# Performance work log

Measured on AMD Instinct MI355X. Metric: run time of the kernel, lower is better.

## Reference

```python
import jax, jax.numpy as jnp
import numpy as np

DIM = 512
HEADS = 8


def setup_inputs() -> dict:
    key = jax.random.key(0)
    ks = jax.random.split(key, 9)
    s = 1.0 / np.sqrt(DIM)
    x = jax.random.normal(ks[0], (2, 4096, DIM), dtype=jnp.float32)
    Wq = jax.random.uniform(ks[1], (DIM, DIM), jnp.float32, -s, s)
    bq = jax.random.uniform(ks[2], (DIM,), jnp.float32, -s, s)
    Wk = jax.random.uniform(ks[3], (DIM, DIM), jnp.float32, -s, s)
    bk = jax.random.uniform(ks[4], (DIM,), jnp.float32, -s, s)
    Wv = jax.random.uniform(ks[5], (DIM, DIM), jnp.float32, -s, s)
    bv = jax.random.uniform(ks[6], (DIM,), jnp.float32, -s, s)
    Wo = jax.random.uniform(ks[7], (DIM, DIM), jnp.float32, -s, s)
    bo = jax.random.uniform(ks[8], (DIM,), jnp.float32, -s, s)
    return {"x": x, "Wq": Wq, "bq": bq, "Wk": Wk, "bk": bk,
            "Wv": Wv, "bv": bv, "Wo": Wo, "bo": bo}


def reference(x, Wq, bq, Wk, bk, Wv, bv, Wo, bo):
    b, t, d = x.shape
    h = HEADS
    dq = d // h
    scale = dq ** -0.5
    # projections: torch Linear is x @ W.T + b
    q = (x @ Wq.T + bq).reshape(b, t, h, dq)
    k = (x @ Wk.T + bk).reshape(b, t, h, dq)
    v = (x @ Wv.T + bv).reshape(b, t, h, dq)
    # attention scores [b, h, t, t] (full O(T^2) matrix, as in the original)
    att = jnp.einsum("bqhd,bkhd->bhqk", q, k) * scale
    att = jax.nn.softmax(att, axis=-1)
    out = jnp.einsum("bhqk,bkhd->bqhd", att, v).reshape(b, t, d)
    return out @ Wo.T + bo
```

## Files before the change

kernel.cpp:

```cpp
#include <hip/hip_runtime.h>

typedef short bf16x8 __attribute__((ext_vector_type(8)));
typedef float f32x4 __attribute__((ext_vector_type(4)));
typedef unsigned u32x2 __attribute__((ext_vector_type(2)));
typedef unsigned u32x4 __attribute__((ext_vector_type(4)));

#define MFMA(a, b, c) __builtin_amdgcn_mfma_f32_16x16x32_bf16((a), (b), (c), 0, 0, 0)

__device__ __forceinline__ unsigned cvtpk(float a, float b) {
    unsigned r;
    asm("v_cvt_pk_bf16_f32 %0, %1, %2" : "=v"(r) : "v"(a), "v"(b));
    return r;
}

__device__ __forceinline__ void gload16(const void* g, void* l) {
    __builtin_amdgcn_global_load_lds(
        (const __attribute__((address_space(1))) unsigned*)g,
        (__attribute__((address_space(3))) unsigned*)l, 16, 0, 0);
}

__global__ __launch_bounds__(256) void cvt_kernel(
    const float* __restrict__ x,
    const float* __restrict__ w0, const float* __restrict__ w1,
    const float* __restrict__ w2, const float* __restrict__ w3,
    unsigned short* __restrict__ xd,
    unsigned short* __restrict__ d0, unsigned short* __restrict__ d1,
    unsigned short* __restrict__ d2, unsigned short* __restrict__ d3)
{
    int bid = blockIdx.x;
    const float* src;
    unsigned short* dst;
    int off;
    if (bid < 4096) { src = x; dst = xd; off = bid; }
    else {
        int s = (bid - 4096) >> 8;
        src = s == 0 ? w0 : (s == 1 ? w1 : (s == 2 ? w2 : w3));
        dst = s == 0 ? d0 : (s == 1 ? d1 : (s == 2 ? d2 : d3));
        off = (bid - 4096) & 255;
    }
    size_t i = ((size_t)off * 256 + threadIdx.x) * 4;
    float4 v = *(const float4*)(src + i);
    uint2 pk;
    pk.x = cvtpk(v.x, v.y);
    pk.y = cvtpk(v.z, v.w);
    *(uint2*)(dst + i) = pk;
}

__global__ __launch_bounds__(512, 6) void qkv_kernel(
    const unsigned short* __restrict__ x,
    const unsigned short* __restrict__ Wq, const float* __restrict__ bq,
    const unsigned short* __restrict__ Wk, const float* __restrict__ bk,
    const unsigned short* __restrict__ Wv, const float* __restrict__ bv,
    unsigned short* __restrict__ qo, unsigned short* __restrict__ ko,
    unsigned short* __restrict__ vo)
{
    __shared__ unsigned short sA[128 * 64];
    __shared__ unsigned short sB[128 * 64];
    const int tid = threadIdx.x;
    const int lane = tid & 63, wid = tid >> 6;
    const int quad = lane >> 4, l15 = lane & 15;
    const int wm = wid >> 2, wn = wid & 3;
    const int by = blockIdx.y;
    const int sel = by >> 2;
    const int n0 = (by & 3) * 128;
    const int m0 = blockIdx.x * 128;
    const unsigned short* W = sel == 0 ? Wq : (sel == 1 ? Wk : Wv);
    const float* bias = sel == 0 ? bq : (sel == 1 ? bk : bv);

    const int gl_r = lane >> 3;
    const int gl_kc = (lane & 7) ^ gl_r;

    f32x4 acc[4][2];
    #pragma unroll
    for (int i = 0; i < 4; i++)
        #pragma unroll
        for (int j = 0; j < 2; j++) {
            f32x4 z = {0.f, 0.f, 0.f, 0.f};
            acc[i][j] = z;
        }

    for (int k0 = 0; k0 < 512; k0 += 64) {
        #pragma unroll
        for (int p = 0; p < 2; p++) {
            int chunk = wid * 2 + p;
            int row = chunk * 8 + gl_r;
            gload16(x + (size_t)(m0 + row) * 512 + k0 + gl_kc * 8,
                    (char*)sA + chunk * 1024);
            gload16(W + (size_t)(n0 + row) * 512 + k0 + gl_kc * 8,
                    (char*)sB + chunk * 1024);
        }
        __asm__ __volatile__("s_waitcnt vmcnt(0)" ::: "memory");
        __syncthreads();
        #pragma unroll
        for (int ks = 0; ks < 2; ks++) {
            bf16x8 af[4], bfr[2];
            #pragma unroll
            for (int i = 0; i < 4; i++) {
                int row = wm * 64 + i * 16 + l15;
                int kc = ks * 4 + quad;
                af[i] = *(const bf16x8*)((const char*)sA + row * 128 + ((kc ^ (row & 7)) << 4));
            }
            #pragma unroll
            for (int j = 0; j < 2; j++) {
                int row = wn * 32 + j * 16 + l15;
                int kc = ks * 4 + quad;
                bfr[j] = *(const bf16x8*)((const char*)sB + row * 128 + ((kc ^ (row & 7)) << 4));
            }
            #pragma unroll
            for (int i = 0; i < 4; i++)
                #pragma unroll
                for (int j = 0; j < 2; j++)
                    acc[i][j] = MFMA(af[i], bfr[j], acc[i][j]);
        }
        __syncthreads();
    }

    float bv2[2];
    #pragma unroll
    for (int j = 0; j < 2; j++) bv2[j] = bias[n0 + wn * 32 + j * 16 + l15];

    if (sel != 1) {
        const float SC = (sel == 0) ? 0.125f * 1.44269504088896f : 1.0f;
        unsigned short* dstT = (sel == 0) ? qo : vo;
        #pragma unroll
        for (int i = 0; i < 4; i++) {
            #pragma unroll
            for (int j = 0; j < 2; j++) {
                int n = n0 + wn * 32 + j * 16 + l15;
                int h = n >> 6, d = n & 63;
                int m = m0 + wm * 64 + i * 16 + quad * 4;
                int b = m >> 12, t = m & 4095;
                uint2 pk;
                pk.x = cvtpk((acc[i][j][0] + bv2[j]) * SC,
                             (acc[i][j][1] + bv2[j]) * SC);
                pk.y = cvtpk((acc[i][j][2] + bv2[j]) * SC,
                             (acc[i][j][3] + bv2[j]) * SC);
                *(uint2*)(dstT + ((size_t)(b * 8 + h) * 64 + d) * 4096 + t) = pk;
            }
        }
    } else {
        #pragma unroll
        for (int i = 0; i < 4; i++) {
            #pragma unroll
            for (int j = 0; j < 2; j++) {
                int n = n0 + wn * 32 + j * 16 + l15;
                int h = n >> 6, d = n & 63;
                int m = m0 + wm * 64 + i * 16 + quad * 4;
                int b = m >> 12, t = m & 4095;
                size_t base2 = ((size_t)(b * 8 + h) * 4096 + t) * 64 + d;
                unsigned p01 = cvtpk(acc[i][j][0] + bv2[j], acc[i][j][1] + bv2[j]);
                unsigned p23 = cvtpk(acc[i][j][2] + bv2[j], acc[i][j][3] + bv2[j]);
                ko[base2]       = (unsigned short)p01;
                ko[base2 + 64]  = (unsigned short)(p01 >> 16);
                ko[base2 + 128] = (unsigned short)p23;
                ko[base2 + 192] = (unsigned short)(p23 >> 16);
            }
        }
    }
}

__global__ __launch_bounds__(512, 4) void attn_kernel(
    const unsigned short* __restrict__ qg, const unsigned short* __restrict__ kg,
    const unsigned short* __restrict__ vtg, unsigned short* __restrict__ og)
{
    __shared__ unsigned char smem[66048];

    const int tid = threadIdx.x;
    const int lane = tid & 63;
    const int w = tid >> 6;
    const int g = tid >> 8;
    const int wg = w & 3;
    const int sw = w & 3;
    const int quad = lane >> 4, l15 = lane & 15;
    const int bh = blockIdx.y;
    const size_t base = (size_t)bh * 4096 * 64;
    const unsigned short* Q = qg + base;
    const unsigned short* K = kg + base;
    const unsigned short* VT = vtg + base;
    const int qt0 = blockIdx.x * 128;

    const int srow = lane >> 3;
    const int skc  = (lane & 7) ^ srow;

    int kLaneOff[2], vLaneOff[2], dKOff[2], dVOff[2];
    #pragma unroll
    for (int p = 0; p < 2; p++) {
        int chunk = wg * 2 + p;
        int row = chunk * 8 + srow;
        kLaneOff[p] = row * 64 + skc * 8;
        vLaneOff[p] = row * 4096 + skc * 8;
        dKOff[p] = g * 8192 + chunk * 1024;
        dVOff[p] = 16384 + g * 8192 + chunk * 1024;
    }

    int okS[4][2], okV[4][2];
    #pragma unroll
    for (int rb = 0; rb < 4; rb++)
        #pragma unroll
        for (int ks = 0; ks < 2; ks++) {
            int row = rb * 16 + l15;
            int kc = ks * 4 + quad;
            int sl = ((kc ^ (row & 7)) << 4);
            okS[rb][ks] = g * 8192 + row * 128 + sl;
            okV[rb][ks] = 16384 + g * 8192 + row * 128 + sl;
        }

    bf16x8 qf[2][2];
    #pragma unroll
    for (int cb = 0; cb < 2; cb++) {
        int t = qt0 + sw * 32 + cb * 16 + l15;
        #pragma unroll
        for (int ks = 0; ks < 2; ks++) {
            bf16x8 v;
            #pragma unroll
            for (int e = 0; e < 8; e++)
                v[e] = (short)Q[(size_t)(ks * 32 + quad * 8 + e) * 4096 + t];
            qf[cb][ks] = v;
        }
    }

    f32x4 ot[4][2];
    #pragma unroll
    for (int i = 0; i < 4; i++)
        #pragma unroll
        for (int cb = 0; cb < 2; cb++) {
            f32x4 z = {0.f, 0.f, 0.f, 0.f};
            ot[i][cb] = z;
        }
    f32x4 ls[2];
    {
        f32x4 z = {0.f, 0.f, 0.f, 0.f};
        ls[0] = z; ls[1] = z;
    }
    const short one_b = (short)0x3F80;
    const bf16x8 ones = {one_b, one_b, one_b, one_b, one_b, one_b, one_b, one_b};

    {
        int kb = g * 64;
        #pragma unroll
        for (int p = 0; p < 2; p++) {
            gload16(K + (size_t)kb * 64 + kLaneOff[p], smem + dKOff[p]);
            gload16(VT + (size_t)kb + vLaneOff[p], smem + dVOff[p]);
        }
    }

    auto do_iter = [&](int it, int bufoff) {
        __asm__ __volatile__("s_waitcnt vmcnt(0)" ::: "memory");
        __syncthreads();

        if (it < 31) {
            int kb = (2 * (it + 1) + g) * 64;
            int od = bufoff ^ 32768;
            #pragma unroll
            for (int p = 0; p < 2; p++) {
                gload16(K + (size_t)kb * 64 + kLaneOff[p], smem + od + dKOff[p]);
                gload16(VT + (size_t)kb + vLaneOff[p], smem + od + dVOff[p]);
            }
        }

        #pragma unroll
        for (int half = 0; half < 2; half++) {
            unsigned xA[2], yA[2], zB[2], wB[2];
            #pragma unroll
            for (int rb2 = 0; rb2 < 2; rb2++) {
                int rb = half * 2 + rb2;
                f32x4 s0 = {0.f, 0.f, 0.f, 0.f};
                f32x4 s1 = {0.f, 0.f, 0.f, 0.f};
                __builtin_amdgcn_s_setprio(1);
                #pragma unroll
                for (int ks = 0; ks < 2; ks++) {
                    bf16x8 ka = *(const bf16x8*)(smem + bufoff + okS[rb][ks]);
                    s0 = MFMA(ka, qf[0][ks], s0);
                    s1 = MFMA(ka, qf[1][ks], s1);
                }
                __builtin_amdgcn_s_setprio(0);
                unsigned e0 = cvtpk(__builtin_amdgcn_exp2f(s0[0]),
                                    __builtin_amdgcn_exp2f(s0[1]));
                unsigned e1 = cvtpk(__builtin_amdgcn_exp2f(s0[2]),
                                    __builtin_amdgcn_exp2f(s0[3]));
                unsigned f0 = cvtpk(__builtin_amdgcn_exp2f(s1[0]),
                                    __builtin_amdgcn_exp2f(s1[1]));
                unsigned f1 = cvtpk(__builtin_amdgcn_exp2f(s1[2]),
                                    __builtin_amdgcn_exp2f(s1[3]));
                if (rb2 == 0) { xA[0] = e0; yA[0] = e1; xA[1] = f0; yA[1] = f1; }
                else          { zB[0] = e0; wB[0] = e1; zB[1] = f0; wB[1] = f1; }
            }

            bf16x8 pf[2];
            #pragma unroll
            for (int cb = 0; cb < 2; cb++) {
                u32x2 s  = __builtin_amdgcn_permlane32_swap(xA[cb], zB[cb], false, false);
                u32x2 t  = __builtin_amdgcn_permlane16_swap(s[0], s[1], false, false);
                u32x2 s2 = __builtin_amdgcn_permlane32_swap(yA[cb], wB[cb], false, false);
                u32x2 t2 = __builtin_amdgcn_permlane16_swap(s2[0], s2[1], false, false);
                u32x4 fr = { t[0], t2[0], t[1], t2[1] };
                pf[cb] = __builtin_bit_cast(bf16x8, fr);
            }

            __builtin_amdgcn_s_setprio(1);
            ls[0] = MFMA(ones, pf[0], ls[0]);
            ls[1] = MFMA(ones, pf[1], ls[1]);
            #pragma unroll
            for (int rbd = 0; rbd < 4; rbd++) {
                bf16x8 vf = *(const bf16x8*)(smem + bufoff + okV[rbd][half]);
                ot[rbd][0] = MFMA(vf, pf[0], ot[rbd][0]);
                ot[rbd][1] = MFMA(vf, pf[1], ot[rbd][1]);
            }
            __builtin_amdgcn_s_setprio(0);
        }
    };

    for (int it2 = 0; it2 < 16; it2++) {
        do_iter(2 * it2, 0);
        do_iter(2 * it2 + 1, 32768);
    }

    float* oc = (float*)smem;
    float* lc = (float*)(smem + 65536);
    if (g == 1) {
        #pragma unroll
        for (int cb = 0; cb < 2; cb++) {
            int qb = sw * 32 + cb * 16 + l15;
            if (quad == 0) lc[qb] = ls[cb][0];
            #pragma unroll
            for (int rbd = 0; rbd < 4; rbd++) {
                int dc = rbd * 4 + quad;
                *(f32x4*)((char*)oc + qb * 256 + ((dc ^ (qb & 15)) << 4)) = ot[rbd][cb];
            }
        }
    }
    __syncthreads();
    if (g == 0) {
        const int b = bh >> 3, h = bh & 7;
        #pragma unroll
        for (int cb = 0; cb < 2; cb++) {
            int qb = sw * 32 + cb * 16 + l15;
            float inv = 1.f / (ls[cb][0] + lc[qb]);
            int q = qt0 + qb;
            #pragma unroll
            for (int rbd = 0; rbd < 4; rbd++) {
                int dc = rbd * 4 + quad;
                f32x4 o2 = *(const f32x4*)((char*)oc + qb * 256 + ((dc ^ (qb & 15)) << 4));
                uint2 pk;
                pk.x = cvtpk((ot[rbd][cb][0] + o2[0]) * inv,
                             (ot[rbd][cb][1] + o2[1]) * inv);
                pk.y = cvtpk((ot[rbd][cb][2] + o2[2]) * inv,
                             (ot[rbd][cb][3] + o2[3]) * inv);
                *(uint2*)(og + ((size_t)(b * 4096 + q) * 512 + h * 64 + rbd * 16 + quad * 4)) = pk;
            }
        }
    }
}

__global__ __launch_bounds__(256) void out_kernel(
    const unsigned short* __restrict__ attn,
    const unsigned short* __restrict__ Wo, const float* __restrict__ bo,
    float* __restrict__ out)
{
    __shared__ unsigned short sA[64 * 64];
    __shared__ unsigned short sB[64 * 64];
    const int tid = threadIdx.x;
    const int lane = tid & 63, wid = tid >> 6;
    const int quad = lane >> 4, l15 = lane & 15;
    const int wm = wid >> 1, wn = wid & 1;
    const int m0 = blockIdx.x * 64;
    const int n0 = blockIdx.y * 64;

    const int gl_r = lane >> 3;
    const int gl_kc = (lane & 7) ^ gl_r;

    f32x4 acc[2][2];
    #pragma unroll
    for (int i = 0; i < 2; i++)
        #pragma unroll
        for (int j = 0; j < 2; j++) {
            f32x4 z = {0.f, 0.f, 0.f, 0.f};
            acc[i][j] = z;
        }

    for (int k0 = 0; k0 < 512; k0 += 64) {
        #pragma unroll
        for (int p = 0; p < 2; p++) {
            int chunk = wid * 2 + p;
            int row = chunk * 8 + gl_r;
            gload16(attn + (size_t)(m0 + row) * 512 + k0 + gl_kc * 8,
                    (char*)sA + chunk * 1024);
            gload16(Wo + (size_t)(n0 + row) * 512 + k0 + gl_kc * 8,
                    (char*)sB + chunk * 1024);
        }
        __asm__ __volatile__("s_waitcnt vmcnt(0)" ::: "memory");
        __syncthreads();
        #pragma unroll
        for (int ks = 0; ks < 2; ks++) {
            bf16x8 af[2], bfr[2];
            #pragma unroll
            for (int i = 0; i < 2; i++) {
                int row = wm * 32 + i * 16 + l15;
                int kc = ks * 4 + quad;
                af[i] = *(const bf16x8*)((const char*)sA + row * 128 + ((kc ^ (row & 7)) << 4));
            }
            #pragma unroll
            for (int j = 0; j < 2; j++) {
                int row = wn * 32 + j * 16 + l15;
                int kc = ks * 4 + quad;
                bfr[j] = *(const bf16x8*)((const char*)sB + row * 128 + ((kc ^ (row & 7)) << 4));
            }
            #pragma unroll
            for (int i = 0; i < 2; i++)
                #pragma unroll
                for (int j = 0; j < 2; j++)
                    acc[i][j] = MFMA(af[i], bfr[j], acc[i][j]);
        }
        __syncthreads();
    }

    float bv2[2];
    #pragma unroll
    for (int j = 0; j < 2; j++) bv2[j] = bo[n0 + wn * 32 + j * 16 + l15];
    #pragma unroll
    for (int i = 0; i < 2; i++) {
        #pragma unroll
        for (int j = 0; j < 2; j++) {
            int n = n0 + wn * 32 + j * 16 + l15;
            #pragma unroll
            for (int r = 0; r < 4; r++) {
                int m = m0 + wm * 32 + i * 16 + quad * 4 + r;
                out[(size_t)m * 512 + n] = acc[i][j][r] + bv2[j];
            }
        }
    }
}

extern "C" void kernel_launch(void* const* d_in, const int* in_sizes, int n_in,
                              void* d_out, int out_size, void* d_ws, size_t ws_size,
                              hipStream_t stream) {
    const float* x  = (const float*)d_in[0];
    const float* Wq = (const float*)d_in[1];
    const float* bq = (const float*)d_in[2];
    const float* Wk = (const float*)d_in[3];
    const float* bk = (const float*)d_in[4];
    const float* Wv = (const float*)d_in[5];
    const float* bv = (const float*)d_in[6];
    const float* Wo = (const float*)d_in[7];
    const float* bo = (const float*)d_in[8];
    unsigned short* ws = (unsigned short*)d_ws;

    const size_t NTOK = (size_t)2 * 4096 * 512;
    const size_t WSZ = (size_t)512 * 512;
    unsigned short* xb  = ws;
    unsigned short* Wqb = ws + NTOK;
    unsigned short* Wkb = Wqb + WSZ;
    unsigned short* Wvb = Wkb + WSZ;
    unsigned short* Wob = Wvb + WSZ;
    unsigned short* q_ws = Wob + WSZ;
    unsigned short* k_ws = q_ws + NTOK;
    unsigned short* v_ws = k_ws + NTOK;
    unsigned short* a_ws = v_ws + NTOK;

    cvt_kernel<<<5120, 256, 0, stream>>>(x, Wq, Wk, Wv, Wo, xb, Wqb, Wkb, Wvb, Wob);
    qkv_kernel<<<dim3(64, 12), 512, 0, stream>>>(xb, Wqb, bq, Wkb, bk, Wvb, bv,
                                                 q_ws, k_ws, v_ws);
    attn_kernel<<<dim3(32, 16), 512, 0, stream>>>(q_ws, k_ws, v_ws, a_ws);
    out_kernel<<<dim3(128, 8), 256, 0, stream>>>(a_ws, Wob, bo,
                                                 (float*)d_out);
}
```

Measured before the change: 186.0 us.

## Restructure attention to 64-query blocks without split-KV reduction

The attention kernel moves from 512-thread blocks that split the key range across two warp groups, each with two 16-query tiles per warp, to 256-thread blocks that handle 64 queries and loop over all 64 key blocks. Each warp now owns a single 16-query tile. This drops the shared-memory cross-group reduction and its extra barrier, halves LDS use, and doubles the grid so more blocks can be resident. In exchange, K/V tiles are reused across half as many queries per load, which doubles K/V traffic from L2/LDS, and each warp has less independent MFMA work to hide latency.

```diff
diff --git a/kernel.cpp b/kernel.cpp
--- a/kernel.cpp
+++ b/kernel.cpp
@@ -159,25 +159,22 @@
     }
 }
 
-__global__ __launch_bounds__(512, 4) void attn_kernel(
+__global__ __launch_bounds__(256, 4) void attn_kernel(
     const unsigned short* __restrict__ qg, const unsigned short* __restrict__ kg,
     const unsigned short* __restrict__ vtg, unsigned short* __restrict__ og)
 {
-    __shared__ unsigned char smem[66048];
+    __shared__ unsigned char smem[32768];
 
     const int tid = threadIdx.x;
     const int lane = tid & 63;
     const int w = tid >> 6;
-    const int g = tid >> 8;
-    const int wg = w & 3;
-    const int sw = w & 3;
     const int quad = lane >> 4, l15 = lane & 15;
     const int bh = blockIdx.y;
     const size_t base = (size_t)bh * 4096 * 64;
     const unsigned short* Q = qg + base;
     const unsigned short* K = kg + base;
     const unsigned short* VT = vtg + base;
-    const int qt0 = blockIdx.x * 128;
+    const int qt0 = blockIdx.x * 64;
 
     const int srow = lane >> 3;
     const int skc  = (lane & 7) ^ srow;
@@ -185,12 +182,12 @@
     int kLaneOff[2], vLaneOff[2], dKOff[2], dVOff[2];
     #pragma unroll
     for (int p = 0; p < 2; p++) {
-        int chunk = wg * 2 + p;
+        int chunk = w * 2 + p;
         int row = chunk * 8 + srow;
         kLaneOff[p] = row * 64 + skc * 8;
         vLaneOff[p] = row * 4096 + skc * 8;
-        dKOff[p] = g * 8192 + chunk * 1024;
-        dVOff[p] = 16384 + g * 8192 + chunk * 1024;
+        dKOff[p] = chunk * 1024;
+        dVOff[p] = 8192 + chunk * 1024;
     }
 
     int okS[4][2], okV[4][2];
@@ -199,58 +196,56 @@
         #pragma unroll
         for (int ks = 0; ks < 2; ks++) {
             int row = rb * 16 + l15;
-            int kc = ks * 4 + quad;
-            int sl = ((kc ^ (row & 7)) << 4);
-            okS[rb][ks] = g * 8192 + row * 128 + sl;
-            okV[rb][ks] = 16384 + g * 8192 + row * 128 + sl;
-        }
-
-    bf16x8 qf[2][2];
-    #pragma unroll
-    for (int cb = 0; cb < 2; cb++) {
-        int t = qt0 + sw * 32 + cb * 16 + l15;
+            okS[rb][ks] = row * 128 + (((ks * 4 + quad) ^ (row & 7)) << 4);
+        }
+    #pragma unroll
+    for (int rbd = 0; rbd < 4; rbd++)
+        #pragma unroll
+        for (int half = 0; half < 2; half++) {
+            int row = rbd * 16 + l15;
+            okV[rbd][half] = 8192 + row * 128 + (((half * 4 + quad) ^ (row & 7)) << 4);
+        }
+
+    bf16x8 qf[2];
+    {
+        int t = qt0 + w * 16 + l15;
         #pragma unroll
         for (int ks = 0; ks < 2; ks++) {
             bf16x8 v;
             #pragma unroll
             for (int e = 0; e < 8; e++)
                 v[e] = (short)Q[(size_t)(ks * 32 + quad * 8 + e) * 4096 + t];
-            qf[cb][ks] = v;
-        }
-    }
-
-    f32x4 ot[4][2];
-    #pragma unroll
-    for (int i = 0; i < 4; i++)
-        #pragma unroll
-        for (int cb = 0; cb < 2; cb++) {
-            f32x4 z = {0.f, 0.f, 0.f, 0.f};
-            ot[i][cb] = z;
-        }
-    f32x4 ls[2];
+            qf[ks] = v;
+        }
+    }
+
+    f32x4 ot[4];
+    #pragma unroll
+    for (int i = 0; i < 4; i++) {
+        f32x4 z = {0.f, 0.f, 0.f, 0.f};
+        ot[i] = z;
+    }
+    f32x4 ls;
     {
         f32x4 z = {0.f, 0.f, 0.f, 0.f};
-        ls[0] = z; ls[1] = z;
+        ls = z;
     }
     const short one_b = (short)0x3F80;
     const bf16x8 ones = {one_b, one_b, one_b, one_b, one_b, one_b, one_b, one_b};
 
-    {
-        int kb = g * 64;
-        #pragma unroll
-        for (int p = 0; p < 2; p++) {
-            gload16(K + (size_t)kb * 64 + kLaneOff[p], smem + dKOff[p]);
-            gload16(VT + (size_t)kb + vLaneOff[p], smem + dVOff[p]);
-        }
+    #pragma unroll
+    for (int p = 0; p < 2; p++) {
+        gload16(K + kLaneOff[p], smem + dKOff[p]);
+        gload16(VT + vLaneOff[p], smem + dVOff[p]);
     }
 
     auto do_iter = [&](int it, int bufoff) {
         __asm__ __volatile__("s_waitcnt vmcnt(0)" ::: "memory");
         __syncthreads();
 
-        if (it < 31) {
-            int kb = (2 * (it + 1) + g) * 64;
-            int od = bufoff ^ 32768;
+        if (it < 63) {
+            int kb = (it + 1) * 64;
+            int od = bufoff ^ 16384;
             #pragma unroll
             for (int p = 0; p < 2; p++) {
                 gload16(K + (size_t)kb * 64 + kLaneOff[p], smem + od + dKOff[p]);
@@ -260,94 +255,59 @@
 
         #pragma unroll
         for (int half = 0; half < 2; half++) {
-            unsigned xA[2], yA[2], zB[2], wB[2];
+            unsigned xA, yA, zB, wB;
             #pragma unroll
             for (int rb2 = 0; rb2 < 2; rb2++) {
                 int rb = half * 2 + rb2;
                 f32x4 s0 = {0.f, 0.f, 0.f, 0.f};
-                f32x4 s1 = {0.f, 0.f, 0.f, 0.f};
                 __builtin_amdgcn_s_setprio(1);
                 #pragma unroll
                 for (int ks = 0; ks < 2; ks++) {
                     bf16x8 ka = *(const bf16x8*)(smem + bufoff + okS[rb][ks]);
-                    s0 = MFMA(ka, qf[0][ks], s0);
-                    s1 = MFMA(ka, qf[1][ks], s1);
+                    s0 = MFMA(ka, qf[ks], s0);
                 }
                 __builtin_amdgcn_s_setprio(0);
                 unsigned e0 = cvtpk(__builtin_amdgcn_exp2f(s0[0]),
                                     __builtin_amdgcn_exp2f(s0[1]));
                 unsigned e1 = cvtpk(__builtin_amdgcn_exp2f(s0[2]),
                                     __builtin_amdgcn_exp2f(s0[3]));
-                unsigned f0 = cvtpk(__builtin_amdgcn_exp2f(s1[0]),
-                                    __builtin_amdgcn_exp2f(s1[1]));
-                unsigned f1 = cvtpk(__builtin_amdgcn_exp2f(s1[2]),
-                                    __builtin_amdgcn_exp2f(s1[3]));
-                if (rb2 == 0) { xA[0] = e0; yA[0] = e1; xA[1] = f0; yA[1] = f1; }
-                else          { zB[0] = e0; wB[0] = e1; zB[1] = f0; wB[1] = f1; }
-            }
-
-            bf16x8 pf[2];
-            #pragma unroll
-            for (int cb = 0; cb < 2; cb++) {
-                u32x2 s  = __builtin_amdgcn_permlane32_swap(xA[cb], zB[cb], false, false);
-                u32x2 t  = __builtin_amdgcn_permlane16_swap(s[0], s[1], false, false);
-                u32x2 s2 = __builtin_amdgcn_permlane32_swap(yA[cb], wB[cb], false, false);
-                u32x2 t2 = __builtin_amdgcn_permlane16_swap(s2[0], s2[1], false, false);
-                u32x4 fr = { t[0], t2[0], t[1], t2[1] };
-                pf[cb] = __builtin_bit_cast(bf16x8, fr);
-            }
+                if (rb2 == 0) { xA = e0; yA = e1; }
+                else          { zB = e0; wB = e1; }
+            }
+
+            u32x2 sa  = __builtin_amdgcn_permlane32_swap(xA, zB, false, false);
+            u32x2 ta  = __builtin_amdgcn_permlane16_swap(sa[0], sa[1], false, false);
+            u32x2 sb  = __builtin_amdgcn_permlane32_swap(yA, wB, false, false);
+            u32x2 tb  = __builtin_amdgcn_permlane16_swap(sb[0], sb[1], false, false);
+            u32x4 fr = { ta[0], tb[0], ta[1], tb[1] };
+            bf16x8 pf = __builtin_bit_cast(bf16x8, fr);
 
             __builtin_amdgcn_s_setprio(1);
-            ls[0] = MFMA(ones, pf[0], ls[0]);
-            ls[1] = MFMA(ones, pf[1], ls[1]);
+            ls = MFMA(ones, pf, ls);
             #pragma unroll
             for (int rbd = 0; rbd < 4; rbd++) {
                 bf16x8 vf = *(const bf16x8*)(smem + bufoff + okV[rbd][half]);
-                ot[rbd][0] = MFMA(vf, pf[0], ot[rbd][0]);
-                ot[rbd][1] = MFMA(vf, pf[1], ot[rbd][1]);
+                ot[rbd] = MFMA(vf, pf, ot[rbd]);
             }
             __builtin_amdgcn_s_setprio(0);
         }
     };
 
-    for (int it2 = 0; it2 < 16; it2++) {
+    for (int it2 = 0; it2 < 32; it2++) {
         do_iter(2 * it2, 0);
-        do_iter(2 * it2 + 1, 32768);
-    }
-
-    float* oc = (float*)smem;
-    float* lc = (float*)(smem + 65536);
-    if (g == 1) {
-        #pragma unroll
-        for (int cb = 0; cb < 2; cb++) {
-            int qb = sw * 32 + cb * 16 + l15;
-            if (quad == 0) lc[qb] = ls[cb][0];
-            #pragma unroll
-            for (int rbd = 0; rbd < 4; rbd++) {
-                int dc = rbd * 4 + quad;
-                *(f32x4*)((char*)oc + qb * 256 + ((dc ^ (qb & 15)) << 4)) = ot[rbd][cb];
-            }
-        }
-    }
-    __syncthreads();
-    if (g == 0) {
+        do_iter(2 * it2 + 1, 16384);
+    }
+
+    {
         const int b = bh >> 3, h = bh & 7;
-        #pragma unroll
-        for (int cb = 0; cb < 2; cb++) {
-            int qb = sw * 32 + cb * 16 + l15;
-            float inv = 1.f / (ls[cb][0] + lc[qb]);
-            int q = qt0 + qb;
-            #pragma unroll
-            for (int rbd = 0; rbd < 4; rbd++) {
-                int dc = rbd * 4 + quad;
-                f32x4 o2 = *(const f32x4*)((char*)oc + qb * 256 + ((dc ^ (qb & 15)) << 4));
-                uint2 pk;
-                pk.x = cvtpk((ot[rbd][cb][0] + o2[0]) * inv,
-                             (ot[rbd][cb][1] + o2[1]) * inv);
-                pk.y = cvtpk((ot[rbd][cb][2] + o2[2]) * inv,
-                             (ot[rbd][cb][3] + o2[3]) * inv);
-                *(uint2*)(og + ((size_t)(b * 4096 + q) * 512 + h * 64 + rbd * 16 + quad * 4)) = pk;
-            }
+        float inv = 1.f / ls[0];
+        int q = qt0 + w * 16 + l15;
+        #pragma unroll
+        for (int rbd = 0; rbd < 4; rbd++) {
+            uint2 pk;
+            pk.x = cvtpk(ot[rbd][0] * inv, ot[rbd][1] * inv);
+            pk.y = cvtpk(ot[rbd][2] * inv, ot[rbd][3] * inv);
+            *(uint2*)(og + ((size_t)(b * 4096 + q) * 512 + h * 64 + rbd * 16 + quad * 4)) = pk;
         }
     }
 }
@@ -460,7 +420,7 @@
     cvt_kernel<<<5120, 256, 0, stream>>>(x, Wq, Wk, Wv, Wo, xb, Wqb, Wkb, Wvb, Wob);
     qkv_kernel<<<dim3(64, 12), 512, 0, stream>>>(xb, Wqb, bq, Wkb, bk, Wvb, bv,
                                                  q_ws, k_ws, v_ws);
-    attn_kernel<<<dim3(32, 16), 512, 0, stream>>>(q_ws, k_ws, v_ws, a_ws);
+    attn_kernel<<<dim3(64, 16), 256, 0, stream>>>(q_ws, k_ws, v_ws, a_ws);
     out_kernel<<<dim3(128, 8), 256, 0, stream>>>(a_ws, Wob, bo,
                                                  (float*)d_out);
 }
```

New measurement: 198.4 us. 6.7% more time.
